# Kernel optimization log

Measured on AMD Instinct MI355X. Metric: run time of the kernel, lower is better.

## Reference

```python
import math
import jax, jax.numpy as jnp
import numpy as np

B, A, T, C, H, WF = 8, 64, 128, 256, 8, 4
EPS = 1e-5


def setup_inputs() -> dict:
    key = jax.random.key(0)
    ks = jax.random.split(key, 16)
    s = 0.02
    inp = {
        "x": jax.random.normal(ks[0], (B, A, T, C), dtype=jnp.float32),
        "mask_x": jax.random.bernoulli(ks[1], 0.1, (B, A, T)),
        "ln1_w": jnp.ones((C,), jnp.float32),
        "ln1_b": jnp.zeros((C,), jnp.float32),
        "qkv_w": jax.random.normal(ks[2], (3 * C, C), jnp.float32) * s,
        "qkv_b": jnp.zeros((3 * C,), jnp.float32),
        "proj_w": jax.random.normal(ks[3], (C, C), jnp.float32) * s,
        "proj_b": jnp.zeros((C,), jnp.float32),
        "ln2_w": jnp.ones((C,), jnp.float32),
        "ln2_b": jnp.zeros((C,), jnp.float32),
        "fc1_w": jax.random.normal(ks[4], (WF * C, C), jnp.float32) * s,
        "fc1_b": jnp.zeros((WF * C,), jnp.float32),
        "fc2_w": jax.random.normal(ks[5], (C, WF * C), jnp.float32) * s,
        "fc2_b": jnp.zeros((C,), jnp.float32),
    }
    return inp


def _layer_norm(v, w, b):
    m = jnp.mean(v, axis=-1, keepdims=True)
    var = jnp.var(v, axis=-1, keepdims=True)
    return (v - m) * jax.lax.rsqrt(var + EPS) * w + b


def reference(x, mask_x, ln1_w, ln1_b, qkv_w, qkv_b, proj_w, proj_b,
              ln2_w, ln2_b, fc1_w, fc1_b, fc2_w, fc2_b):
    b, a, t, c = x.shape
    h = H
    d = c // h
    # x = ln_1(x); residual is taken AFTER ln_1, matching the torch code
    x1 = _layer_norm(x, ln1_w, ln1_b)
    qkv = x1 @ qkv_w.T + qkv_b  # (B,A,T,3C)
    q, k, v = jnp.split(qkv, 3, axis=-1)
    q = q.reshape(b, a, t, h, d)
    k = k.reshape(b, a, t, h, d)
    v = v.reshape(b, a, t, h, d)
    # attention across time, per agent: (B,A,H,T,T)
    att = jnp.einsum('bathd,bashd->bahts', q, k) * (1.0 / math.sqrt(d))
    mask_val = -jnp.finfo(jnp.float32).max
    # mask broadcast over query rows (torch repeats mask over key dim too,
    # but the pattern masks entire query rows t)
    att = jnp.where(mask_x[:, :, None, :, None], mask_val, att)
    att = jax.nn.softmax(att, axis=-1)
    y = jnp.einsum('bahts,bashd->bathd', att, v).reshape(b, a, t, c)
    y = y @ proj_w.T + proj_b
    x2 = x1 + y
    x3 = _layer_norm(x2, ln2_w, ln2_b)
    mlp = jax.nn.gelu(x3 @ fc1_w.T + fc1_b, approximate=False) @ fc2_w.T + fc2_b
    return x3 + mlp
```

## Files before the change

kernel.cpp:

```cpp
#include <hip/hip_runtime.h>
#include <hip/hip_bf16.h>

typedef unsigned short u16;
typedef unsigned int   u32;

static constexpr int Bc = 8, Ac = 64, Tc = 128, Cc = 256, Hc = 8;
static constexpr int NROW = Bc * Ac * Tc;
static constexpr int DH = Cc / Hc;

__device__ __forceinline__ float bf2f(u16 h) {
    u32 u = ((u32)h) << 16; float f; __builtin_memcpy(&f, &u, 4); return f;
}
__device__ __forceinline__ u16 f2bf(float f) {
    u32 u; __builtin_memcpy(&u, &f, 4);
    u += 0x7fffu + ((u >> 16) & 1u);
    return (u16)(u >> 16);
}

__device__ __forceinline__ float gelu_f(float x) {
    return x / (1.0f + __expf(-1.702f * x));
}

typedef __attribute__((ext_vector_type(8))) short  short8v;
typedef __attribute__((ext_vector_type(4))) float  float4v;

__device__ __forceinline__ void gload16(const void* g, const void* lds) {
    __builtin_amdgcn_global_load_lds(
        (const __attribute__((address_space(1))) void*)g,
        (__attribute__((address_space(3))) void*)lds, 16, 0, 0);
}

#define MFMA16(a, b, c) __builtin_amdgcn_mfma_f32_16x16x32_bf16((a), (b), (c), 0, 0, 0)

__global__ void cast4_kernel(const float* __restrict__ a, int na,
                             const float* __restrict__ b, int nb,
                             const float* __restrict__ c, int nc,
                             const float* __restrict__ d, int nd,
                             u16* oa, u16* ob, u16* oc, u16* od) {
    int i = blockIdx.x * 256 + threadIdx.x;
    if (i < na) { oa[i] = f2bf(a[i]); return; }
    i -= na;
    if (i < nb) { ob[i] = f2bf(b[i]); return; }
    i -= nb;
    if (i < nc) { oc[i] = f2bf(c[i]); return; }
    i -= nc;
    if (i < nd) { od[i] = f2bf(d[i]); }
}

__global__ __launch_bounds__(256) void ln_f32(const float* __restrict__ in,
        const float* __restrict__ w, const float* __restrict__ b,
        u16* __restrict__ out) {
    int row  = blockIdx.x * 4 + (threadIdx.x >> 6);
    int lane = threadIdx.x & 63;
    const float* rp = in + (size_t)row * Cc + lane * 4;
    float4 v = *(const float4*)rp;
    float s  = v.x + v.y + v.z + v.w;
    float sq = v.x * v.x + v.y * v.y + v.z * v.z + v.w * v.w;
    for (int off = 32; off; off >>= 1) { s += __shfl_xor(s, off); sq += __shfl_xor(sq, off); }
    float mean = s * (1.f / Cc);
    float rs = rsqrtf(sq * (1.f / Cc) - mean * mean + 1e-5f);
    int c0 = lane * 4;
    float vv[4] = {v.x, v.y, v.z, v.w};
    ushort4 ov;
    ov.x = f2bf((vv[0] - mean) * rs * w[c0 + 0] + b[c0 + 0]);
    ov.y = f2bf((vv[1] - mean) * rs * w[c0 + 1] + b[c0 + 1]);
    ov.z = f2bf((vv[2] - mean) * rs * w[c0 + 2] + b[c0 + 2]);
    ov.w = f2bf((vv[3] - mean) * rs * w[c0 + 3] + b[c0 + 3]);
    *(ushort4*)(out + (size_t)row * Cc + c0) = ov;
}

__global__ __launch_bounds__(256) void ln_bf16(const u16* __restrict__ in,
        const float* __restrict__ w, const float* __restrict__ b,
        u16* __restrict__ out) {
    int row  = blockIdx.x * 4 + (threadIdx.x >> 6);
    int lane = threadIdx.x & 63;
    const u16* rp = in + (size_t)row * Cc + lane * 4;
    ushort4 hv = *(const ushort4*)rp;
    float vv[4] = {bf2f(hv.x), bf2f(hv.y), bf2f(hv.z), bf2f(hv.w)};
    float s = vv[0] + vv[1] + vv[2] + vv[3];
    float sq = vv[0]*vv[0] + vv[1]*vv[1] + vv[2]*vv[2] + vv[3]*vv[3];
    for (int off = 32; off; off >>= 1) { s += __shfl_xor(s, off); sq += __shfl_xor(sq, off); }
    float mean = s * (1.f / Cc);
    float rs = rsqrtf(sq * (1.f / Cc) - mean * mean + 1e-5f);
    int c0 = lane * 4;
    ushort4 ov;
    ov.x = f2bf((vv[0] - mean) * rs * w[c0 + 0] + b[c0 + 0]);
    ov.y = f2bf((vv[1] - mean) * rs * w[c0 + 1] + b[c0 + 1]);
    ov.z = f2bf((vv[2] - mean) * rs * w[c0 + 2] + b[c0 + 2]);
    ov.w = f2bf((vv[3] - mean) * rs * w[c0 + 3] + b[c0 + 3]);
    *(ushort4*)(out + (size_t)row * Cc + c0) = ov;
}

template<int K, int EPI>
__global__ __launch_bounds__(256) void gemm128p(
        const u16* __restrict__ X, const u16* __restrict__ W,
        const float* __restrict__ bias,
        u16* __restrict__ outb, float* __restrict__ outf,
        const u16* __restrict__ res, int Nf, int nbn) {
    constexpr int NK = K / 32;
    __shared__ __align__(16) u16 smem[24576];
    u16* lA = smem;
    u16* lB = smem + 12288;
    const int nwg = gridDim.x;
    const int q8  = nwg >> 3;
    const int lid = (blockIdx.x & 7) * q8 + (blockIdx.x >> 3);
    const int bn  = (lid % nbn) * 128;
    const int bm  = (lid / nbn) * 128;
    const int tid = threadIdx.x, lane = tid & 63, wave = tid >> 6;
    const int wr = (wave >> 1) * 64, wc = (wave & 1) * 64;
    const int lr = lane & 15, lg = lane >> 4;

    const u16* xsrc[2]; const u16* wsrc[2]; int ldso[2];
    #pragma unroll
    for (int qq = 0; qq < 2; qq++) {
        const int cbase = wave * 128 + qq * 64;
        const int c   = cbase + lane;
        const int row = c >> 2, p = c & 3;
        const int gc  = p ^ ((row >> 1) & 3);
        xsrc[qq] = X + (size_t)(bm + row) * K + gc * 8;
        wsrc[qq] = W + (size_t)(bn + row) * K + gc * 8;
        ldso[qq] = cbase * 8;
    }
    auto stage = [&](int k0, int buf) {
        #pragma unroll
        for (int qq = 0; qq < 2; qq++) {
            gload16(xsrc[qq] + k0, lA + buf * 4096 + ldso[qq]);
            gload16(wsrc[qq] + k0, lB + buf * 4096 + ldso[qq]);
        }
    };

    stage(0, 0);
    stage(32, 1);

    const int rchunk = (lg ^ ((lr >> 1) & 3)) * 8;

    float4v acc[4][4] = {};
    #pragma unroll
    for (int k = 0; k < NK; ++k) {
        if (k + 1 < NK) asm volatile("s_waitcnt vmcnt(4)" ::: "memory");
        else            asm volatile("s_waitcnt vmcnt(0)" ::: "memory");
        __builtin_amdgcn_s_barrier();
        if (k + 2 < NK) stage((k + 2) * 32, (k + 2) % 3);
        const int cur = k % 3;
        short8v a[4], b[4];
        #pragma unroll
        for (int i = 0; i < 4; i++)
            a[i] = *(const short8v*)&lB[cur * 4096 + (wc + i * 16 + lr) * 32 + rchunk];
        #pragma unroll
        for (int j = 0; j < 4; j++)
            b[j] = *(const short8v*)&lA[cur * 4096 + (wr + j * 16 + lr) * 32 + rchunk];
        #pragma unroll
        for (int i = 0; i < 4; i++)
            #pragma unroll
            for (int j = 0; j < 4; j++)
                acc[i][j] = MFMA16(a[i], b[j], acc[i][j]);
    }

    if (EPI == 3) {
        #pragma unroll
        for (int i = 0; i < 4; i++) {
            const int n0 = bn + wc + i * 16 + lg * 4;
            const float4 bv = *(const float4*)&bias[n0];
            #pragma unroll
            for (int j = 0; j < 4; j++) {
                const int m = bm + wr + j * 16 + lr;
                const size_t o0 = (size_t)m * Nf + n0;
                ushort4 rv = *(const ushort4*)(res + o0);
                float4 o;
                o.x = acc[i][j][0] + bv.x + bf2f(rv.x);
                o.y = acc[i][j][1] + bv.y + bf2f(rv.y);
                o.z = acc[i][j][2] + bv.z + bf2f(rv.z);
                o.w = acc[i][j][3] + bv.w + bf2f(rv.w);
                *(float4*)(outf + o0) = o;
            }
        }
    } else {
        __syncthreads();
        u16* ot = smem;
        #pragma unroll
        for (int i = 0; i < 4; i++) {
            const int n0l = wc + i * 16 + lg * 4;
            const float4 bv = *(const float4*)&bias[bn + n0l];
            #pragma unroll
            for (int j = 0; j < 4; j++) {
                const int ml = wr + j * 16 + lr;
                float v0 = acc[i][j][0] + bv.x;
                float v1 = acc[i][j][1] + bv.y;
                float v2 = acc[i][j][2] + bv.z;
                float v3 = acc[i][j][3] + bv.w;
                if (EPI == 1) {
                    const size_t o0 = (size_t)(bm + ml) * Nf + bn + n0l;
                    ushort4 rv = *(const ushort4*)(res + o0);
                    v0 += bf2f(rv.x); v1 += bf2f(rv.y); v2 += bf2f(rv.z); v3 += bf2f(rv.w);
                }
                if (EPI == 2) {
                    v0 = gelu_f(v0); v1 = gelu_f(v1); v2 = gelu_f(v2); v3 = gelu_f(v3);
                }
                ushort4 o;
                o.x = f2bf(v0); o.y = f2bf(v1); o.z = f2bf(v2); o.w = f2bf(v3);
                *(ushort4*)&ot[ml * 136 + n0l] = o;
            }
        }
        __syncthreads();
        #pragma unroll
        for (int i2 = 0; i2 < 8; i2++) {
            const int c   = i2 * 256 + tid;
            const int row = c >> 4, ch = c & 15;
            *(uint4*)(outb + (size_t)(bm + row) * Nf + bn + ch * 8) =
                *(const uint4*)&ot[row * 136 + ch * 8];
        }
    }
}

__global__ __launch_bounds__(256) void attn_mfma_h(
        const u16* __restrict__ qkv, const unsigned char* __restrict__ mask,
        u16* __restrict__ out) {
    __shared__ u16 sk[128][32];
    __shared__ u16 svt[32][136];
    __shared__ u16 sp[4][32][136];
    __shared__ unsigned char smask[128];
    const int blk = blockIdx.x;
    const int h   = blk & (Hc - 1);
    const int ba  = blk >> 3;
    const size_t rowbase = (size_t)ba * Tc;
    const int tid  = threadIdx.x;
    const int lane = tid & 63;
    const int wave = tid >> 6;
    const int wq0  = wave * 32;
    const int lrow = lane & 15, lg = lane >> 4;
    if (tid < 128) smask[tid] = mask[rowbase + tid];

    const float scale  = 0.17677669529663687f;
    const float inv128 = 1.0f / 128.0f;
    const float4v zero4 = {0.f, 0.f, 0.f, 0.f};

    {
        const int r = tid >> 1, half = tid & 1;
        const u16* gbase = qkv + (rowbase + r) * 768 + h * 32 + half * 16;
        uint4 k0 = *(const uint4*)(gbase + 256);
        uint4 k1 = *(const uint4*)(gbase + 256 + 8);
        *(uint4*)&sk[r][half * 16]     = k0;
        *(uint4*)&sk[r][half * 16 + 8] = k1;
        uint4 v0 = *(const uint4*)(gbase + 512);
        uint4 v1 = *(const uint4*)(gbase + 512 + 8);
        u16 vt[16];
        *(uint4*)&vt[0] = v0; *(uint4*)&vt[8] = v1;
        #pragma unroll
        for (int e = 0; e < 16; e++) svt[half * 16 + e][r] = vt[e];
    }
    __syncthreads();

    short8v a0, a1;
    {
        const u16* qp0 = qkv + (rowbase + wq0 + lrow) * 768 + h * 32 + lg * 8;
        const u16* qp1 = qp0 + 16 * 768;
        a0 = *(const short8v*)qp0;
        a1 = *(const short8v*)qp1;
    }
    float4v s_acc[2][8];
    #pragma unroll
    for (int j = 0; j < 8; j++) {
        short8v bj = *(const short8v*)&sk[j * 16 + lrow][lg * 8];
        s_acc[0][j] = MFMA16(a0, bj, zero4);
        s_acc[1][j] = MFMA16(a1, bj, zero4);
    }

    #pragma unroll
    for (int i = 0; i < 2; i++) {
        #pragma unroll
        for (int r = 0; r < 4; r++) {
            float m = s_acc[i][0][r];
            #pragma unroll
            for (int j = 1; j < 8; j++) m = fmaxf(m, s_acc[i][j][r]);
            #pragma unroll
            for (int off = 1; off < 16; off <<= 1) m = fmaxf(m, __shfl_xor(m, off));
            float sum = 0.f;
            #pragma unroll
            for (int j = 0; j < 8; j++) {
                float e = __expf((s_acc[i][j][r] - m) * scale);
                sum += e;
                s_acc[i][j][r] = e;
            }
            #pragma unroll
            for (int off = 1; off < 16; off <<= 1) sum += __shfl_xor(sum, off);
            const int qloc = i * 16 + lg * 4 + r;
            const bool mk = smask[wq0 + qloc] != 0;
            const float invs = 1.f / sum;
            #pragma unroll
            for (int j = 0; j < 8; j++) {
                float pv = mk ? inv128 : s_acc[i][j][r] * invs;
                sp[wave][qloc][j * 16 + lrow] = f2bf(pv);
            }
        }
    }

    float4v o_acc[2][2] = {};
    #pragma unroll
    for (int t = 0; t < 4; t++) {
        short8v pa0 = *(const short8v*)&sp[wave][lrow][t * 32 + lg * 8];
        short8v pa1 = *(const short8v*)&sp[wave][16 + lrow][t * 32 + lg * 8];
        short8v vb0 = *(const short8v*)&svt[lrow][t * 32 + lg * 8];
        short8v vb1 = *(const short8v*)&svt[16 + lrow][t * 32 + lg * 8];
        o_acc[0][0] = MFMA16(pa0, vb0, o_acc[0][0]);
        o_acc[0][1] = MFMA16(pa0, vb1, o_acc[0][1]);
        o_acc[1][0] = MFMA16(pa1, vb0, o_acc[1][0]);
        o_acc[1][1] = MFMA16(pa1, vb1, o_acc[1][1]);
    }

    #pragma unroll
    for (int i = 0; i < 2; i++)
        #pragma unroll
        for (int n = 0; n < 2; n++)
            #pragma unroll
            for (int r = 0; r < 4; r++) {
                size_t row = rowbase + wq0 + i * 16 + lg * 4 + r;
                int col = h * 32 + n * 16 + lrow;
                out[row * 256 + col] = f2bf(o_acc[i][n][r]);
            }
}

extern "C" void kernel_launch(void* const* d_in, const int* in_sizes, int n_in,
                              void* d_out, int out_size, void* d_ws, size_t ws_size,
                              hipStream_t stream) {
    const float* x      = (const float*)d_in[0];
    const unsigned char* mask = (const unsigned char*)d_in[1];
    const float* ln1_w  = (const float*)d_in[2];
    const float* ln1_b  = (const float*)d_in[3];
    const float* qkv_w  = (const float*)d_in[4];
    const float* qkv_b  = (const float*)d_in[5];
    const float* proj_w = (const float*)d_in[6];
    const float* proj_b = (const float*)d_in[7];
    const float* ln2_w  = (const float*)d_in[8];
    const float* ln2_b  = (const float*)d_in[9];
    const float* fc1_w  = (const float*)d_in[10];
    const float* fc1_b  = (const float*)d_in[11];
    const float* fc2_w  = (const float*)d_in[12];
    const float* fc2_b  = (const float*)d_in[13];
    float* out = (float*)d_out;

    char* ws = (char*)d_ws;
    size_t off = 0;
    auto alloc = [&](size_t elems) -> u16* {
        u16* p = (u16*)(ws + off);
        off += ((elems * 2 + 255) / 256) * 256;
        return p;
    };
    u16* wqb  = alloc(768 * 256);
    u16* wpb  = alloc(256 * 256);
    u16* w1b  = alloc(1024 * 256);
    u16* w2b  = alloc(256 * 1024);
    u16* x1b  = alloc((size_t)NROW * Cc);
    u16* qkvb = alloc((size_t)NROW * 3 * Cc);
    u16* attb = alloc((size_t)NROW * Cc);
    u16* x2b  = alloc((size_t)NROW * Cc);
    u16* hb   = qkvb;
    u16* x3b  = x1b;

    cast4_kernel<<<(786432 + 255) / 256, 256, 0, stream>>>(
        qkv_w, 196608, proj_w, 65536, fc1_w, 262144, fc2_w, 262144,
        wqb, wpb, w1b, w2b);
    ln_f32<<<NROW / 4, 256, 0, stream>>>(x, ln1_w, ln1_b, x1b);
    gemm128p<256, 0><<<512 * 6, 256, 0, stream>>>(
        x1b, wqb, qkv_b, qkvb, nullptr, nullptr, 768, 6);
    attn_mfma_h<<<Bc * Ac * Hc, 256, 0, stream>>>(qkvb, mask, attb);
    gemm128p<256, 1><<<512 * 2, 256, 0, stream>>>(
        attb, wpb, proj_b, x2b, nullptr, x1b, 256, 2);
    ln_bf16<<<NROW / 4, 256, 0, stream>>>(x2b, ln2_w, ln2_b, x3b);
    gemm128p<256, 2><<<512 * 8, 256, 0, stream>>>(
        x3b, w1b, fc1_b, hb, nullptr, nullptr, 1024, 8);
    gemm128p<1024, 3><<<512 * 2, 256, 0, stream>>>(
        hb, w2b, fc2_b, nullptr, out, x3b, 256, 2);
}
```

Before: 280.6 us.

## Fuse projection GEMM with residual add and LayerNorm into one kernel

Replaces the proj GEMM (128x128 tiles, residual epilogue) plus the separate ln_bf16 kernel with one proj_ln kernel whose block computes a full 128x256 row tile. This lets the LayerNorm statistics be reduced in registers and shared memory directly from the accumulators. It removes the x2 bf16 round trip through global memory and one kernel launch. The cost is a grid of only 512 blocks, twice the accumulator registers per thread and more shared memory, which lowers occupancy for this stage.

```diff
diff --git a/kernel.cpp b/kernel.cpp
--- a/kernel.cpp
+++ b/kernel.cpp
@@ -69,28 +69,6 @@
     *(ushort4*)(out + (size_t)row * Cc + c0) = ov;
 }
 
-__global__ __launch_bounds__(256) void ln_bf16(const u16* __restrict__ in,
-        const float* __restrict__ w, const float* __restrict__ b,
-        u16* __restrict__ out) {
-    int row  = blockIdx.x * 4 + (threadIdx.x >> 6);
-    int lane = threadIdx.x & 63;
-    const u16* rp = in + (size_t)row * Cc + lane * 4;
-    ushort4 hv = *(const ushort4*)rp;
-    float vv[4] = {bf2f(hv.x), bf2f(hv.y), bf2f(hv.z), bf2f(hv.w)};
-    float s = vv[0] + vv[1] + vv[2] + vv[3];
-    float sq = vv[0]*vv[0] + vv[1]*vv[1] + vv[2]*vv[2] + vv[3]*vv[3];
-    for (int off = 32; off; off >>= 1) { s += __shfl_xor(s, off); sq += __shfl_xor(sq, off); }
-    float mean = s * (1.f / Cc);
-    float rs = rsqrtf(sq * (1.f / Cc) - mean * mean + 1e-5f);
-    int c0 = lane * 4;
-    ushort4 ov;
-    ov.x = f2bf((vv[0] - mean) * rs * w[c0 + 0] + b[c0 + 0]);
-    ov.y = f2bf((vv[1] - mean) * rs * w[c0 + 1] + b[c0 + 1]);
-    ov.z = f2bf((vv[2] - mean) * rs * w[c0 + 2] + b[c0 + 2]);
-    ov.w = f2bf((vv[3] - mean) * rs * w[c0 + 3] + b[c0 + 3]);
-    *(ushort4*)(out + (size_t)row * Cc + c0) = ov;
-}
-
 template<int K, int EPI>
 __global__ __launch_bounds__(256) void gemm128p(
         const u16* __restrict__ X, const u16* __restrict__ W,
@@ -188,11 +166,6 @@
                 float v1 = acc[i][j][1] + bv.y;
                 float v2 = acc[i][j][2] + bv.z;
                 float v3 = acc[i][j][3] + bv.w;
-                if (EPI == 1) {
-                    const size_t o0 = (size_t)(bm + ml) * Nf + bn + n0l;
-                    ushort4 rv = *(const ushort4*)(res + o0);
-                    v0 += bf2f(rv.x); v1 += bf2f(rv.y); v2 += bf2f(rv.z); v3 += bf2f(rv.w);
-                }
                 if (EPI == 2) {
                     v0 = gelu_f(v0); v1 = gelu_f(v1); v2 = gelu_f(v2); v3 = gelu_f(v3);
                 }
@@ -209,6 +182,154 @@
             *(uint4*)(outb + (size_t)(bm + row) * Nf + bn + ch * 8) =
                 *(const uint4*)&ot[row * 136 + ch * 8];
         }
+    }
+}
+
+__global__ __launch_bounds__(256) void proj_ln(
+        const u16* __restrict__ X, const u16* __restrict__ W,
+        const float* __restrict__ bias, const u16* __restrict__ res,
+        const float* __restrict__ lnw, const float* __restrict__ lnb,
+        u16* __restrict__ out) {
+    constexpr int K = 256, NK = 8;
+    __shared__ __align__(16) u16 smem[36864];
+    u16* lA = smem;
+    u16* lB = smem + 12288;
+    const int nwg = gridDim.x;
+    const int q8  = nwg >> 3;
+    const int lid = (blockIdx.x & 7) * q8 + (blockIdx.x >> 3);
+    const int bm  = lid * 128;
+    const int tid = threadIdx.x, lane = tid & 63, wave = tid >> 6;
+    const int wr = (wave >> 1) * 64, wc = (wave & 1) * 128;
+    const int lr = lane & 15, lg = lane >> 4;
+
+    const u16* xsrc[2]; int ldsoA[2];
+    #pragma unroll
+    for (int qq = 0; qq < 2; qq++) {
+        const int cbase = wave * 128 + qq * 64;
+        const int c = cbase + lane;
+        const int row = c >> 2, p = c & 3;
+        const int gc = p ^ ((row >> 1) & 3);
+        xsrc[qq] = X + (size_t)(bm + row) * K + gc * 8;
+        ldsoA[qq] = cbase * 8;
+    }
+    const u16* wsrc[4]; int ldsoB[4];
+    #pragma unroll
+    for (int qq = 0; qq < 4; qq++) {
+        const int cbase = wave * 256 + qq * 64;
+        const int c = cbase + lane;
+        const int row = c >> 2, p = c & 3;
+        const int gc = p ^ ((row >> 1) & 3);
+        wsrc[qq] = W + (size_t)row * K + gc * 8;
+        ldsoB[qq] = cbase * 8;
+    }
+    auto stage = [&](int k0, int buf) {
+        #pragma unroll
+        for (int qq = 0; qq < 2; qq++)
+            gload16(xsrc[qq] + k0, lA + buf * 4096 + ldsoA[qq]);
+        #pragma unroll
+        for (int qq = 0; qq < 4; qq++)
+            gload16(wsrc[qq] + k0, lB + buf * 8192 + ldsoB[qq]);
+    };
+    stage(0, 0);
+    stage(32, 1);
+
+    const int rchunk = (lg ^ ((lr >> 1) & 3)) * 8;
+
+    float4v acc[8][4] = {};
+    #pragma unroll
+    for (int k = 0; k < NK; ++k) {
+        if (k + 1 < NK) asm volatile("s_waitcnt vmcnt(6)" ::: "memory");
+        else            asm volatile("s_waitcnt vmcnt(0)" ::: "memory");
+        __builtin_amdgcn_s_barrier();
+        if (k + 2 < NK) stage((k + 2) * 32, (k + 2) % 3);
+        const int cur = k % 3;
+        short8v a[8], b[4];
+        #pragma unroll
+        for (int i = 0; i < 8; i++)
+            a[i] = *(const short8v*)&lB[cur * 8192 + (wc + i * 16 + lr) * 32 + rchunk];
+        #pragma unroll
+        for (int j = 0; j < 4; j++)
+            b[j] = *(const short8v*)&lA[cur * 4096 + (wr + j * 16 + lr) * 32 + rchunk];
+        #pragma unroll
+        for (int i = 0; i < 8; i++)
+            #pragma unroll
+            for (int j = 0; j < 4; j++)
+                acc[i][j] = MFMA16(a[i], b[j], acc[i][j]);
+    }
+
+    #pragma unroll
+    for (int i = 0; i < 8; i++) {
+        const int n0 = wc + i * 16 + lg * 4;
+        const float4 bv = *(const float4*)&bias[n0];
+        #pragma unroll
+        for (int j = 0; j < 4; j++) {
+            const int m = bm + wr + j * 16 + lr;
+            ushort4 rv = *(const ushort4*)(res + (size_t)m * 256 + n0);
+            acc[i][j][0] += bv.x + bf2f(rv.x);
+            acc[i][j][1] += bv.y + bf2f(rv.y);
+            acc[i][j][2] += bv.z + bf2f(rv.z);
+            acc[i][j][3] += bv.w + bf2f(rv.w);
+        }
+    }
+    float ps[4], pq[4];
+    #pragma unroll
+    for (int j = 0; j < 4; j++) {
+        float s = 0.f, q = 0.f;
+        #pragma unroll
+        for (int i = 0; i < 8; i++)
+            #pragma unroll
+            for (int r = 0; r < 4; r++) { float v = acc[i][j][r]; s += v; q += v * v; }
+        s += __shfl_xor(s, 16); s += __shfl_xor(s, 32);
+        q += __shfl_xor(q, 16); q += __shfl_xor(q, 32);
+        ps[j] = s; pq[j] = q;
+    }
+    __syncthreads();
+    float* pbuf = (float*)smem;
+    const int half = wave & 1;
+    #pragma unroll
+    for (int j = 0; j < 4; j++) {
+        const int rml = wr + j * 16 + lr;
+        if (lg == 0) {
+            pbuf[(rml * 2 + half) * 2 + 0] = ps[j];
+            pbuf[(rml * 2 + half) * 2 + 1] = pq[j];
+        }
+    }
+    __syncthreads();
+    float mean_[4], rs_[4];
+    #pragma unroll
+    for (int j = 0; j < 4; j++) {
+        const int rml = wr + j * 16 + lr;
+        float s = pbuf[(rml * 2 + 0) * 2 + 0] + pbuf[(rml * 2 + 1) * 2 + 0];
+        float q = pbuf[(rml * 2 + 0) * 2 + 1] + pbuf[(rml * 2 + 1) * 2 + 1];
+        float mean = s * (1.f / 256.f);
+        mean_[j] = mean;
+        rs_[j] = rsqrtf(q * (1.f / 256.f) - mean * mean + 1e-5f);
+    }
+    __syncthreads();
+    u16* ot = smem;
+    #pragma unroll
+    for (int i = 0; i < 8; i++) {
+        const int n0 = wc + i * 16 + lg * 4;
+        const float4 w4 = *(const float4*)&lnw[n0];
+        const float4 b4 = *(const float4*)&lnb[n0];
+        #pragma unroll
+        for (int j = 0; j < 4; j++) {
+            const int rml = wr + j * 16 + lr;
+            ushort4 o;
+            o.x = f2bf((acc[i][j][0] - mean_[j]) * rs_[j] * w4.x + b4.x);
+            o.y = f2bf((acc[i][j][1] - mean_[j]) * rs_[j] * w4.y + b4.y);
+            o.z = f2bf((acc[i][j][2] - mean_[j]) * rs_[j] * w4.z + b4.z);
+            o.w = f2bf((acc[i][j][3] - mean_[j]) * rs_[j] * w4.w + b4.w);
+            *(ushort4*)&ot[rml * 264 + n0] = o;
+        }
+    }
+    __syncthreads();
+    #pragma unroll
+    for (int i2 = 0; i2 < 16; i2++) {
+        const int c = i2 * 256 + tid;
+        const int row = c >> 5, ch = c & 31;
+        *(uint4*)(out + (size_t)(bm + row) * 256 + ch * 8) =
+            *(const uint4*)&ot[row * 264 + ch * 8];
     }
 }
 
@@ -352,9 +473,8 @@
     u16* x1b  = alloc((size_t)NROW * Cc);
     u16* qkvb = alloc((size_t)NROW * 3 * Cc);
     u16* attb = alloc((size_t)NROW * Cc);
-    u16* x2b  = alloc((size_t)NROW * Cc);
+    u16* x3b  = alloc((size_t)NROW * Cc);
     u16* hb   = qkvb;
-    u16* x3b  = x1b;
 
     cast4_kernel<<<(786432 + 255) / 256, 256, 0, stream>>>(
         qkv_w, 196608, proj_w, 65536, fc1_w, 262144, fc2_w, 262144,
@@ -363,9 +483,8 @@
     gemm128p<256, 0><<<512 * 6, 256, 0, stream>>>(
         x1b, wqb, qkv_b, qkvb, nullptr, nullptr, 768, 6);
     attn_mfma_h<<<Bc * Ac * Hc, 256, 0, stream>>>(qkvb, mask, attb);
-    gemm128p<256, 1><<<512 * 2, 256, 0, stream>>>(
-        attb, wpb, proj_b, x2b, nullptr, x1b, 256, 2);
-    ln_bf16<<<NROW / 4, 256, 0, stream>>>(x2b, ln2_w, ln2_b, x3b);
+    proj_ln<<<512, 256, 0, stream>>>(
+        attb, wpb, proj_b, x1b, ln2_w, ln2_b, x3b);
     gemm128p<256, 2><<<512 * 8, 256, 0, stream>>>(
         x3b, w1b, fc1_b, hb, nullptr, nullptr, 1024, 8);
     gemm128p<1024, 3><<<512 * 2, 256, 0, stream>>>(
```

New measurement: 272.7 us. 2.8% less time.
